# Optimization experiments

Hardware: AMD Instinct MI355X
Metric: run time of the kernel (lower is better)

The kernel has to match this reference:

```python
import jax, jax.numpy as jnp
import numpy as np

# unit conversions: Hartree -> kcal/mol, Bohr -> Ang (as in schnetpack convert_units)
ENERGY_CONVERSION = 627.5094740631
POSITION_CONVERSION = 0.529177210903
DAMPING = 0.1
DAMP_FACTOR = DAMPING * ENERGY_CONVERSION / POSITION_CONVERSION ** 2  # scalar on diag

M = 8192        # molecules
N_PER = 32      # atoms per molecule (uniform -> ragged loop collapses to batched matvec)
D = 3 * N_PER   # hessian block dim = 96
N_TOT = M * N_PER


def setup_inputs() -> dict:
    key = jax.random.key(0)
    k1, k2 = jax.random.split(key)
    ns = jax.random.normal(k1, (N_TOT, 3), dtype=jnp.float32)
    # row-stacked per-molecule hessian blocks: [M*D, D]
    hess = jax.random.normal(k2, (M * D, D), dtype=jnp.float32)
    idx_m = jnp.repeat(jnp.arange(M, dtype=jnp.int64), N_PER)  # per-atom molecule id, sorted
    n_atoms = jnp.full((M,), N_PER, dtype=jnp.int64)
    return {"ns": ns, "hess": hess, "idx_m": idx_m, "n_atoms": n_atoms}


def reference(ns, hess, idx_m, n_atoms):
    # idx_m is sorted repeats of arange(M) with uniform molecule size, so the
    # per-molecule boolean-mask gathers are equivalent to reshapes.
    m = n_atoms.shape[0]
    d = 3 * (ns.shape[0] // m)                    # 3 * n_per
    x = ns.reshape(m, d)                          # flattened newton step per molecule
    H = hess.reshape(m, d, d)                     # per-molecule hessian blocks
    # f = H @ ns + (damping_factor * I) @ ns
    f = jnp.einsum('mij,mj->mi', H, x) + DAMP_FACTOR * x
    return f.reshape(-1, 3)                       # [N_tot, 3] forces
```

## Files before the change

kernel.cpp:

```cpp
#include <hip/hip_runtime.h>


#define D_DIM   96
#define QROW    24
#define MPB     2
#define ROWS    (D_DIM * MPB)
#define QBLK    (ROWS * QROW)
#define BLOCK   256
#define ITERS   (QBLK / BLOCK)
#define PSTRIDE 25

typedef float f4 __attribute__((ext_vector_type(4), aligned(16)));

__global__ __launch_bounds__(BLOCK)
void force_agg_kernel(const float* __restrict__ hess,
                      const float* __restrict__ ns,
                      float* __restrict__ out)
{
    __shared__ float partial[ROWS * PSTRIDE];

    const int t = threadIdx.x;
    const f4* __restrict__ H4 = reinterpret_cast<const f4*>(hess)
                              + (size_t)blockIdx.x * QBLK;
    const f4* __restrict__ X4 = reinterpret_cast<const f4*>(ns)
                              + (size_t)blockIdx.x * (ROWS / 4);

#pragma unroll
    for (int i = 0; i < ITERS; ++i) {
        const int q   = t + i * BLOCK;
        const int row = q / QROW;
        const int k   = q - row * QROW;
        const int xi  = k + ((row >= D_DIM) ? QROW : 0);
        const f4 h  = __builtin_nontemporal_load(H4 + q);
        const f4 xv = X4[xi];
        partial[row * PSTRIDE + k] = h.x * xv.x + h.y * xv.y
                                   + h.z * xv.z + h.w * xv.w;
    }
    __syncthreads();

    if (t < ROWS) {
        float s0 = 0.f, s1 = 0.f, s2 = 0.f, s3 = 0.f;
        const float* p = &partial[t * PSTRIDE];
#pragma unroll
        for (int k = 0; k < 6; ++k) {
            s0 += p[k];
            s1 += p[k + 6];
            s2 += p[k + 12];
            s3 += p[k + 18];
        }
        const float DAMP =
            (float)(0.1 * 627.5094740631 / (0.529177210903 * 0.529177210903));
        const float xt = ns[(size_t)blockIdx.x * ROWS + t];
        __builtin_nontemporal_store((s0 + s1) + (s2 + s3) + DAMP * xt,
                                    out + (size_t)blockIdx.x * ROWS + t);
    }
}

extern "C" void kernel_launch(void* const* d_in, const int* in_sizes, int n_in,
                              void* d_out, int out_size, void* d_ws, size_t ws_size,
                              hipStream_t stream)
{
    const float* ns   = (const float*)d_in[0];
    const float* hess = (const float*)d_in[1];
    float* out = (float*)d_out;

    const int M = in_sizes[0] / D_DIM;
    force_agg_kernel<<<M / MPB, BLOCK, 0, stream>>>(hess, ns, out);
}
```

Measured before the change: 380.1 us.

## Process four tiles per block with register prefetch and double-buffered shared memory

Each block now handles four consecutive two-molecule tiles. The Hessian loads for the next tile are issued into registers while the current tile's partial products are reduced, and a pair of alternating shared-memory buffers lets that overlap happen with a single barrier per tile. The aim is to keep more memory requests in flight per block and to spread launch overhead over more work. In exchange the grid is four times smaller (1024 blocks), register pressure rises with the 18-element f4 array, and the launch bounds hint now asks for higher occupancy.

```diff
diff --git a/kernel.cpp b/kernel.cpp
--- a/kernel.cpp
+++ b/kernel.cpp
@@ -9,50 +9,73 @@
 #define BLOCK   256
 #define ITERS   (QBLK / BLOCK)
 #define PSTRIDE 25
+#define TPB     4
 
 typedef float f4 __attribute__((ext_vector_type(4), aligned(16)));
 
-__global__ __launch_bounds__(BLOCK)
+__global__ __launch_bounds__(BLOCK, 4)
 void force_agg_kernel(const float* __restrict__ hess,
                       const float* __restrict__ ns,
                       float* __restrict__ out)
 {
-    __shared__ float partial[ROWS * PSTRIDE];
+    __shared__ float partial[2][ROWS * PSTRIDE];
 
-    const int t = threadIdx.x;
-    const f4* __restrict__ H4 = reinterpret_cast<const f4*>(hess)
-                              + (size_t)blockIdx.x * QBLK;
-    const f4* __restrict__ X4 = reinterpret_cast<const f4*>(ns)
-                              + (size_t)blockIdx.x * (ROWS / 4);
+    const int t     = threadIdx.x;
+    const int tile0 = blockIdx.x * TPB;
+
+    const f4* __restrict__ H4 = reinterpret_cast<const f4*>(hess);
+    const f4* __restrict__ X4 = reinterpret_cast<const f4*>(ns);
+
+    f4 h[ITERS];
+    {
+        const f4* p = H4 + (size_t)tile0 * QBLK + t;
+#pragma unroll
+        for (int i = 0; i < ITERS; ++i)
+            h[i] = __builtin_nontemporal_load(p + i * BLOCK);
+    }
 
 #pragma unroll
-    for (int i = 0; i < ITERS; ++i) {
-        const int q   = t + i * BLOCK;
-        const int row = q / QROW;
-        const int k   = q - row * QROW;
-        const int xi  = k + ((row >= D_DIM) ? QROW : 0);
-        const f4 h  = __builtin_nontemporal_load(H4 + q);
-        const f4 xv = X4[xi];
-        partial[row * PSTRIDE + k] = h.x * xv.x + h.y * xv.y
-                                   + h.z * xv.z + h.w * xv.w;
-    }
-    __syncthreads();
+    for (int j = 0; j < TPB; ++j) {
+        const int tile = tile0 + j;
+        float* buf = partial[j & 1];
+        const f4* Xt = X4 + (size_t)tile * (ROWS / 4);
 
-    if (t < ROWS) {
-        float s0 = 0.f, s1 = 0.f, s2 = 0.f, s3 = 0.f;
-        const float* p = &partial[t * PSTRIDE];
 #pragma unroll
-        for (int k = 0; k < 6; ++k) {
-            s0 += p[k];
-            s1 += p[k + 6];
-            s2 += p[k + 12];
-            s3 += p[k + 18];
+        for (int i = 0; i < ITERS; ++i) {
+            const int q   = t + i * BLOCK;
+            const int row = q / QROW;
+            const int k   = q - row * QROW;
+            const int xi  = k + ((row >= D_DIM) ? QROW : 0);
+            const f4 xv = Xt[xi];
+            buf[row * PSTRIDE + k] = h[i].x * xv.x + h[i].y * xv.y
+                                   + h[i].z * xv.z + h[i].w * xv.w;
         }
-        const float DAMP =
-            (float)(0.1 * 627.5094740631 / (0.529177210903 * 0.529177210903));
-        const float xt = ns[(size_t)blockIdx.x * ROWS + t];
-        __builtin_nontemporal_store((s0 + s1) + (s2 + s3) + DAMP * xt,
-                                    out + (size_t)blockIdx.x * ROWS + t);
+
+        if (j + 1 < TPB) {
+            const f4* p = H4 + (size_t)(tile + 1) * QBLK + t;
+#pragma unroll
+            for (int i = 0; i < ITERS; ++i)
+                h[i] = __builtin_nontemporal_load(p + i * BLOCK);
+        }
+
+        __syncthreads();
+
+        if (t < ROWS) {
+            float s0 = 0.f, s1 = 0.f, s2 = 0.f, s3 = 0.f;
+            const float* pp = &buf[t * PSTRIDE];
+#pragma unroll
+            for (int k = 0; k < 6; ++k) {
+                s0 += pp[k];
+                s1 += pp[k + 6];
+                s2 += pp[k + 12];
+                s3 += pp[k + 18];
+            }
+            const float DAMP =
+                (float)(0.1 * 627.5094740631 / (0.529177210903 * 0.529177210903));
+            const float xt = ns[(size_t)tile * ROWS + t];
+            __builtin_nontemporal_store((s0 + s1) + (s2 + s3) + DAMP * xt,
+                                        out + (size_t)tile * ROWS + t);
+        }
     }
 }
 
@@ -64,6 +87,7 @@
     const float* hess = (const float*)d_in[1];
     float* out = (float*)d_out;
 
-    const int M = in_sizes[0] / D_DIM;
-    force_agg_kernel<<<M / MPB, BLOCK, 0, stream>>>(hess, ns, out);
+    const int M     = in_sizes[0] / D_DIM;
+    const int tiles = M / MPB;
+    force_agg_kernel<<<tiles / TPB, BLOCK, 0, stream>>>(hess, ns, out);
 }
```

New measurement: 410.1 us. 1.08x slower.
